# Kernel tuning notes

Hardware: AMD Instinct MI355X
Metric: run time of the kernel (lower is better)

## Reference

```python
import jax, jax.numpy as jnp
from jax import lax
import numpy as np

K = 32          # PyG radius_graph default max_num_neighbors
NEG = -1e9      # mask fill for max-aggregation


def _gather(a, i):  # a [N,C], i [...,] int -> a[i]
    return a[i]


def radius_knn(pos, r):
    # pos [B,N,3] -> (idx [B,N,K], valid [B,N,K]) nearest-K within radius r, self excluded
    sq = jnp.sum(pos * pos, -1)                                   # [B,N]
    d2 = sq[:, :, None] + sq[:, None, :] - 2.0 * jnp.einsum('bnc,bmc->bnm', pos, pos)
    N = pos.shape[1]
    d2 = d2 + jnp.eye(N, dtype=pos.dtype) * 1e9                    # exclude self-loops
    neg, idx = lax.top_k(-d2, K)
    valid = (-neg) <= r * r
    return idx, valid


def fps(pos, n):
    # iterative farthest point sampling, deterministic start at index 0; pos [B,N,3] -> idx [B,n]
    def one(p):
        mind0 = jnp.sum((p - p[0]) ** 2, -1)
        def step(mind, _):
            i = jnp.argmax(mind)
            nd = jnp.sum((p - p[i]) ** 2, -1)
            return jnp.minimum(mind, nd), i
        _, idxs = lax.scan(step, mind0, None, length=n - 1)
        return jnp.concatenate([jnp.zeros((1,), jnp.int32), idxs.astype(jnp.int32)])
    return jax.vmap(one)(pos)


def point_conv(x, pos, idx, valid, W1, b1, W2, b2):
    # PyG PointNetConv: msg = local_nn(concat(x_j, pos_j - pos_i)), max-aggregate
    g = jax.vmap(_gather)
    rel = g(pos, idx) - pos[:, :, None, :]                         # [B,N,K,3]
    feat = rel if x is None else jnp.concatenate([g(x, idx), rel], -1)
    h = jax.nn.relu(feat @ W1 + b1) @ W2 + b2                      # [B,N,K,C]
    h = jnp.where(valid[..., None], h, NEG)
    return jnp.max(h, axis=2)                                      # [B,N,C]


def _forward(pos, W1a, b1a, W1b, b1b, W2a, b2a, W2b, b2b, W3a, b3a, W3b, b3b,
             Wc1, bc1, Wc2, bc2, Wc3, bc3, Wd1, bd1, Wd2, bd2):
    take = jax.vmap(_gather)
    B, N, _ = pos.shape
    idx, v = radius_knn(pos, 0.2)
    x = jax.nn.relu(point_conv(None, pos, idx, v, W1a, b1a, W1b, b1b))
    fi = fps(pos, N // 2)
    x, pos = take(x, fi), take(pos, fi)
    idx, v = radius_knn(pos, 0.4)
    x = jax.nn.relu(point_conv(x, pos, idx, v, W2a, b2a, W2b, b2b))
    fi = fps(pos, N // 8)
    x, pos = take(x, fi), take(pos, fi)
    idx, v = radius_knn(pos, 1.0)
    x = jax.nn.relu(point_conv(x, pos, idx, v, W3a, b3a, W3b, b3b))
    feat = jnp.max(x, axis=1)                                      # global max pool [B,256]
    h = jax.nn.relu(feat @ Wc1 + bc1)
    h = jax.nn.relu(h @ Wc2 + bc2)                                 # dropout is identity in eval
    logits = h @ Wc3 + bc3
    h2 = jax.nn.relu(feat @ Wd1 + bd1)
    d = h2 @ Wd2 + bd2
    return jax.nn.log_softmax(logits, axis=-1), jax.nn.log_softmax(d, axis=-1)


def setup_inputs() -> dict:
    key = jax.random.key(0)
    ks = jax.random.split(key, 32)
    def lin(k, fin, fout):
        kw, kb = jax.random.split(k)
        s = 1.0 / np.sqrt(fin)
        return (jax.random.uniform(kw, (fin, fout), jnp.float32, -s, s),
                jax.random.uniform(kb, (fout,), jnp.float32, -s, s))
    inp = {'pos': jax.random.uniform(ks[0], (8, 4096, 3), jnp.float32)}
    names = [('W1a','b1a',3,64),('W1b','b1b',64,64),('W2a','b2a',67,128),('W2b','b2b',128,128),
             ('W3a','b3a',131,256),('W3b','b3b',256,256),('Wc1','bc1',256,256),('Wc2','bc2',256,256),
             ('Wc3','bc3',256,40),('Wd1','bd1',256,256),('Wd2','bd2',256,2)]
    for i, (wn, bn, fin, fout) in enumerate(names):
        W, b = lin(ks[i + 1], fin, fout)
        inp[wn], inp[bn] = W, b
    return inp


def reference(pos, W1a, b1a, W1b, b1b, W2a, b2a, W2b, b2b, W3a, b3a, W3b, b3b,
              Wc1, bc1, Wc2, bc2, Wc3, bc3, Wd1, bd1, Wd2, bd2):
    return _forward(pos, W1a, b1a, W1b, b1b, W2a, b2a, W2b, b2b, W3a, b3a, W3b, b3b,
                    Wc1, bc1, Wc2, bc2, Wc3, bc3, Wd1, bd1, Wd2, bd2)
```

## Files before the change

### kernel.cpp

```cpp
#include <hip/hip_runtime.h>


#define NB 8

__device__ __forceinline__ unsigned obits(float f) {
  unsigned u = __float_as_uint(f);
  return (u & 0x80000000u) ? ~u : (u | 0x80000000u);
}

static constexpr int CAND = 1024;

template<int CTRL>
__device__ __forceinline__ unsigned long long dpp_max_step(unsigned long long v) {
  const int lo = (int)(unsigned)(v & 0xffffffffull);
  const int hi = (int)(unsigned)(v >> 32);
  const unsigned nlo = (unsigned)__builtin_amdgcn_update_dpp(lo, lo, CTRL, 0xf, 0xf, false);
  const unsigned nhi = (unsigned)__builtin_amdgcn_update_dpp(hi, hi, CTRL, 0xf, 0xf, false);
  const unsigned long long nv = ((unsigned long long)nhi << 32) | nlo;
  return (nv > v) ? nv : v;
}

__device__ __forceinline__ unsigned wave_iscan_add(unsigned x) {
  x += (unsigned)__builtin_amdgcn_update_dpp(0, (int)x, 0x111, 0xf, 0xf, true);
  x += (unsigned)__builtin_amdgcn_update_dpp(0, (int)x, 0x112, 0xf, 0xf, true);
  x += (unsigned)__builtin_amdgcn_update_dpp(0, (int)x, 0x114, 0xf, 0xf, true);
  x += (unsigned)__builtin_amdgcn_update_dpp(0, (int)x, 0x118, 0xf, 0xf, true);
  x += (unsigned)__builtin_amdgcn_update_dpp(0, (int)x, 0x142, 0xa, 0xf, true);
  x += (unsigned)__builtin_amdgcn_update_dpp(0, (int)x, 0x143, 0xc, 0xf, true);
  return x;
}

__device__ __forceinline__ unsigned long long u64max(unsigned long long a,
                                                    unsigned long long b) {
  return (b > a) ? b : a;
}

__device__ __forceinline__ void set_wave_prio_hi() {
#if __has_builtin(__builtin_amdgcn_s_setprio)
  __builtin_amdgcn_s_setprio(3);
#endif
}

template<int N, int NOUT, int T>
__device__ __forceinline__ void fps_body(char* sm, const float* __restrict__ pb,
                                         int* __restrict__ fi, int b) {
  constexpr int P = N / T;
  constexpr int NW = T / 64;
  int4* sPosI = (int4*)sm;
  int*  sfi   = (int*)(sm + (size_t)N * 16);
  unsigned long long* sKey =
      (unsigned long long*)(sm + (size_t)N * 16 + NOUT * 4);
  const int tid = threadIdx.x, wid = tid >> 6, lane = tid & 63;
  set_wave_prio_hi();
  int ix[P], iy[P], iz[P];
  unsigned long long mind[P];
  for (int t = tid; t < N; t += T) {
    sPosI[t] = make_int4((int)(pb[3*t]   * 8388608.f),
                         (int)(pb[3*t+1] * 8388608.f),
                         (int)(pb[3*t+2] * 8388608.f), 0);
  }
  __syncthreads();
  const int x0 = sPosI[0].x, y0 = sPosI[0].y, z0 = sPosI[0].z;
  const int invBase = 4095 - tid * P;
  unsigned long long bv;
  {
    unsigned long long tv[P];
#pragma unroll
    for (int e = 0; e < P; e++) {
      const int j = tid * P + e;
      const int4 p4 = sPosI[j];
      ix[e] = p4.x; iy[e] = p4.y; iz[e] = p4.z;
      const long long dx = p4.x - x0, dy = p4.y - y0, dz = p4.z - z0;
      const unsigned long long d2 =
          (unsigned long long)(dx * dx + dy * dy + dz * dz);
      const unsigned long long k = (d2 << 12) | (unsigned)(invBase - e);
      mind[e] = k; tv[e] = k;
    }
#pragma unroll
    for (int s = 1; s < P; s <<= 1)
#pragma unroll
      for (int e = 0; e + s < P; e += 2 * s)
        if (tv[e + s] > tv[e]) tv[e] = tv[e + s];
    bv = tv[0];
  }
  if (tid == 0) sfi[0] = 0;
  for (int t = 1; t < NOUT; t++) {
    unsigned long long v = bv;
    v = dpp_max_step<0x111>(v);
    v = dpp_max_step<0x112>(v);
    v = dpp_max_step<0x114>(v);
    v = dpp_max_step<0x118>(v);
    v = dpp_max_step<0x142>(v);
    v = dpp_max_step<0x143>(v);
    const int pp = t & 1;
    if (lane == 63) sKey[pp * NW + wid] = v;
    __syncthreads();
    unsigned long long best;
    if (NW == 8) {
      unsigned long long k0 = sKey[pp*8+0], k1 = sKey[pp*8+1],
                         k2 = sKey[pp*8+2], k3 = sKey[pp*8+3],
                         k4 = sKey[pp*8+4], k5 = sKey[pp*8+5],
                         k6 = sKey[pp*8+6], k7 = sKey[pp*8+7];
      k0 = u64max(k0, k1); k2 = u64max(k2, k3);
      k4 = u64max(k4, k5); k6 = u64max(k6, k7);
      k0 = u64max(k0, k2); k4 = u64max(k4, k6);
      best = u64max(k0, k4);
    } else {
      unsigned long long k0 = sKey[pp*NW+0];
#pragma unroll
      for (int w2 = 1; w2 < NW; w2++) k0 = u64max(k0, sKey[pp*NW+w2]);
      best = k0;
    }
    const int ii = 4095 - (int)(best & 0xFFFull);
    if (tid == 0) sfi[t] = ii;
    const int4 wc = sPosI[ii];
    unsigned long long tv[P];
#pragma unroll
    for (int e = 0; e < P; e++) {
      const long long dx = ix[e] - wc.x, dy = iy[e] - wc.y, dz = iz[e] - wc.z;
      const unsigned long long nd =
          (unsigned long long)(dx * dx + dy * dy + dz * dz);
      const unsigned long long nk = (nd << 12) | (unsigned)(invBase - e);
      unsigned long long mk = mind[e];
      mk = (nk < mk) ? nk : mk;
      mind[e] = mk;
      tv[e] = mk;
    }
#pragma unroll
    for (int s = 1; s < P; s <<= 1)
#pragma unroll
      for (int e = 0; e + s < P; e += 2 * s)
        if (tv[e + s] > tv[e]) tv[e] = tv[e + s];
    bv = tv[0];
  }
  __syncthreads();
  for (int t = tid; t < NOUT; t += T) fi[(size_t)b * NOUT + t] = sfi[t];
}

template<int N, int H, int C, bool HASX, bool FOLDMAX, int T>
__device__ __forceinline__ void knnconv_body(
    char* sm, const float* __restrict__ pb, int b, int i,
    const float* __restrict__ U, const float* __restrict__ Wrel,
    const float* __restrict__ b1, const float* __restrict__ W2,
    const float* __restrict__ b2, float* __restrict__ out, double rr) {
  constexpr int HCHUNK = (C == 64) ? 64 : (C == 128 ? 32 : 16);
  constexpr int STR = HCHUNK + 4;
  constexpr int NW = T / 64;
  constexpr int EPK = 32 / NW;
  constexpr int BPT = 2048 / T;
  constexpr int KNNFRONT = N * 8 + 13312;
  constexpr int CONVFRONT = 32 * H * 4 + C * STR * 4 + NW * C * 4;
  constexpr int FRONT = (KNNFRONT > CONVFRONT) ? KNNFRONT : CONVFRONT;
  double*   d2s     = (double*)sm;
  unsigned* hist    = (unsigned*)(sm + N * 8);
  int*      candIdx = (int*)(sm + N * 8 + 8192);
  unsigned* sWT     = (unsigned*)(sm + N * 8 + 12288);
  float* h1s  = (float*)sm;
  float* sW2T = (float*)(sm + 32 * H * 4);
  float* sRed = (float*)(sm + 32 * H * 4 + C * STR * 4);
  int*   snbr = (int*)(sm + FRONT);
  float* rel  = (float*)(sm + FRONT + 128);
  int*   pcnt = (int*)(sm + FRONT + 128 + 384);
  int*   pbin = pcnt + 1;
  const int tid = threadIdx.x;

  const double xi = pb[3*i], yi = pb[3*i+1], zi = pb[3*i+2];
  const double si = (xi*xi + yi*yi) + zi*zi;
  for (int t = tid; t < 2048; t += T) hist[t] = 0u;
  if (tid == 0) *pcnt = 0;
  __syncthreads();
  for (int j = tid; j < N; j += T) {
    double xj = pb[3*j], yj = pb[3*j+1], zj = pb[3*j+2];
    double sj = (xj*xj + yj*yj) + zj*zj;
    double dt = (xi*xj + yi*yj) + zi*zj;
    double d2 = (si + sj) - 2.0*dt;
    if (j == i) d2 += 1e9;
    d2s[j] = d2;
    atomicAdd(&hist[obits((float)d2) >> 21], 1u);
  }
  __syncthreads();
  unsigned lsum = 0;
  const int base = tid * BPT;
#pragma unroll
  for (int q = 0; q < BPT; q++) lsum += hist[base + q];
  const unsigned isc = wave_iscan_add(lsum);
  if ((tid & 63) == 63) sWT[tid >> 6] = isc;
  __syncthreads();
  {
    const int wid = tid >> 6;
    unsigned offs = 0;
#pragma unroll
    for (int w2 = 0; w2 < NW; w2++) offs += (w2 < wid) ? sWT[w2] : 0u;
    const unsigned incl = isc + offs, excl = incl - lsum;
    if (excl < 32u && incl >= 32u) {
      unsigned c = excl;
      for (int q = 0; q < BPT; q++) {
        c += hist[base + q];
        if (c >= 32u) { *pbin = base + q; break; }
      }
    }
  }
  __syncthreads();
  const int binT = *pbin;
  for (int j = tid; j < N; j += T) {
    if ((int)(obits((float)d2s[j]) >> 21) <= binT) {
      int p = atomicAdd(pcnt, 1);
      if (p < CAND) candIdx[p] = j;
    }
  }
  __syncthreads();
  const int M = min(*pcnt, CAND);
  for (int c = tid; c < M; c += T) {
    const int j = candIdx[c];
    const double d = d2s[j];
    int rank = 0;
    for (int e = 0; e < M; e++) {
      const int j2 = candIdx[e];
      const double de = d2s[j2];
      rank += (de < d || (de == d && j2 < j)) ? 1 : 0;
    }
    if (rank < 32) snbr[rank] = (d <= rr) ? j : -1;
  }
  __syncthreads();

  if (tid < 32) {
    const int j = snbr[tid];
    float rx = 0.f, ry = 0.f, rz = 0.f;
    if (j >= 0) {
      rx = pb[3*j]   - pb[3*i];
      ry = pb[3*j+1] - pb[3*i+1];
      rz = pb[3*j+2] - pb[3*i+2];
    }
    rel[tid*3+0] = rx; rel[tid*3+1] = ry; rel[tid*3+2] = rz;
  }
  __syncthreads();

  constexpr int QPK = H / 4;
  for (int qi = tid; qi < 32 * QPK; qi += T) {
    const int k = qi / QPK, h0 = (qi - k * QPK) * 4;
    const int j = snbr[k];
    float4 v = make_float4(0.f, 0.f, 0.f, 0.f);
    if (j >= 0) {
      float4 a = HASX ? *(const float4*)&U[((size_t)b * N + j) * H + h0]
                      : *(const float4*)&b1[h0];
      const float rx = rel[k*3], ry = rel[k*3+1], rz = rel[k*3+2];
      const float4 w0 = *(const float4*)&Wrel[h0];
      const float4 w1 = *(const float4*)&Wrel[H + h0];
      const float4 w2 = *(const float4*)&Wrel[2 * H + h0];
      a.x += rx * w0.x + ry * w1.x + rz * w2.x;
      a.y += rx * w0.y + ry * w1.y + rz * w2.y;
      a.z += rx * w0.z + ry * w1.z + rz * w2.z;
      a.w += rx * w0.w + ry * w1.w + rz * w2.w;
      v = make_float4(fmaxf(a.x, 0.f), fmaxf(a.y, 0.f),
                      fmaxf(a.z, 0.f), fmaxf(a.w, 0.f));
    }
    *(float4*)&h1s[k * H + h0] = v;
  }
  const int cc = tid & 63;
  const int kk = tid >> 6;
  constexpr int CC = C / 64;
  float acc[EPK][CC];
#pragma unroll
  for (int e = 0; e < EPK; e++)
#pragma unroll
    for (int q = 0; q < CC; q++) acc[e][q] = 0.f;
  for (int hc = 0; hc < H; hc += HCHUNK) {
    __syncthreads();
    for (int idx = tid; idx < HCHUNK * C; idx += T) {
      const int hh = idx / C, c = idx - hh * C;
      sW2T[c * STR + hh] = W2[(size_t)(hc + hh) * C + c];
    }
    __syncthreads();
    for (int hh0 = 0; hh0 < HCHUNK; hh0 += 4) {
      float4 wv[CC];
#pragma unroll
      for (int q = 0; q < CC; q++)
        wv[q] = *(const float4*)&sW2T[(cc + q * 64) * STR + hh0];
#pragma unroll
      for (int e = 0; e < EPK; e++) {
        const float4 hv = *(const float4*)&h1s[(kk + e * NW) * H + hc + hh0];
#pragma unroll
        for (int q = 0; q < CC; q++) {
          acc[e][q] += hv.x * wv[q].x;
          acc[e][q] += hv.y * wv[q].y;
          acc[e][q] += hv.z * wv[q].z;
          acc[e][q] += hv.w * wv[q].w;
        }
      }
    }
  }
  float m[CC];
#pragma unroll
  for (int q = 0; q < CC; q++) m[q] = -1e9f;
#pragma unroll
  for (int e = 0; e < EPK; e++) {
    if (snbr[kk + e * NW] >= 0) {
#pragma unroll
      for (int q = 0; q < CC; q++) m[q] = fmaxf(m[q], acc[e][q]);
    }
  }
#pragma unroll
  for (int q = 0; q < CC; q++) sRed[kk * C + cc + q * 64] = m[q];
  __syncthreads();
  if (kk == 0) {
#pragma unroll
    for (int q = 0; q < CC; q++) {
      const int c = cc + q * 64;
      float mm = sRed[c];
#pragma unroll
      for (int w2 = 1; w2 < NW; w2++) mm = fmaxf(mm, sRed[w2 * C + c]);
      const float o = (mm > -5e8f) ? (mm + b2[c]) : -1e9f;
      const float r = fmaxf(o, 0.f);
      if (FOLDMAX) {
        atomicMax((int*)&out[b * C + c], __float_as_int(r));
      } else {
        out[((size_t)b * N + i) * C + c] = r;
      }
    }
  }
}

template<int N, int NOUT, int H, int C, bool HASX, int SMSIZE>
__device__ __forceinline__ void stage_fused_impl(
    const float* pos, double rr, int* fi, const float* U, const float* Wrel,
    const float* b1, const float* W2, const float* b2, float* out, char* sm) {
  if (blockIdx.x < NB) {
    fps_body<N, NOUT, 512>(sm, pos + (size_t)blockIdx.x * N * 3, fi, blockIdx.x);
  } else {
    const int row = blockIdx.x - NB;
    const int b = row / N;
    const int i = row - b * N;
    knnconv_body<N, H, C, HASX, false, 512>(sm, pos + (size_t)b * N * 3, b, i,
                                            U, Wrel, b1, W2, b2, out, rr);
  }
}

__global__ __launch_bounds__(512, 2)
void stage1_kernel(const float* __restrict__ pos, double rr, int* __restrict__ fi,
                   const float* __restrict__ Wrel, const float* __restrict__ b1,
                   const float* __restrict__ W2, const float* __restrict__ b2,
                   float* __restrict__ out) {
  __shared__ __align__(16) char sm[73856];
  stage_fused_impl<4096, 2048, 64, 64, false, 73856>(
      pos, rr, fi, nullptr, Wrel, b1, W2, b2, out, sm);
}

__global__ __launch_bounds__(512, 2)
void stage2_kernel(const float* __restrict__ pos, double rr, int* __restrict__ fi,
                   const float* __restrict__ U, const float* __restrict__ Wrel,
                   const float* __restrict__ b1, const float* __restrict__ W2,
                   const float* __restrict__ b2, float* __restrict__ out) {
  __shared__ __align__(16) char sm[39440];
  stage_fused_impl<2048, 512, 128, 128, true, 39440>(
      pos, rr, fi, U, Wrel, b1, W2, b2, out, sm);
}

__global__ __launch_bounds__(512)
void stage3_kernel(const float* __restrict__ pos, double rr,
                   const float* __restrict__ U, const float* __restrict__ Wrel,
                   const float* __restrict__ b1, const float* __restrict__ W2,
                   const float* __restrict__ b2, float* __restrict__ feat) {
  __shared__ __align__(16) char sm[61968];
  const int b = blockIdx.x / 512;
  const int i = blockIdx.x - b * 512;
  knnconv_body<512, 256, 256, true, true, 512>(sm, pos + (size_t)b * 512 * 3,
                                               b, i, U, Wrel, b1, W2, b2,
                                               feat, rr);
}

template<int CIN, int HH>
__global__ __launch_bounds__(HH)
void gp_kernel(const float* __restrict__ X, const float* __restrict__ posPrev,
               const int* __restrict__ fi, int Nprev, int M,
               const float* __restrict__ W, const float* __restrict__ bias,
               float* __restrict__ U, float* __restrict__ posDst) {
  const int row = blockIdx.x;
  const int b = row / M;
  const int tid = threadIdx.x;
  const int j = fi[row];
  __shared__ float sx[CIN];
  if (tid < CIN) sx[tid] = X[((size_t)b * Nprev + j) * CIN + tid];
  if (tid < 3) posDst[(size_t)row * 3 + tid] = posPrev[((size_t)b * Nprev + j) * 3 + tid];
  __syncthreads();
  float a = bias[tid];
  for (int f = 0; f < CIN; f++) a = fmaf(sx[f], W[f * HH + tid], a);
  U[(size_t)row * HH + tid] = a;
}

__global__ __launch_bounds__(256) void head_kernel(
    const float* __restrict__ feat,
    const float* __restrict__ Wc1, const float* __restrict__ bc1,
    const float* __restrict__ Wc2, const float* __restrict__ bc2,
    const float* __restrict__ Wc3, const float* __restrict__ bc3,
    const float* __restrict__ Wd1, const float* __restrict__ bd1,
    const float* __restrict__ Wd2, const float* __restrict__ bd2,
    float* __restrict__ out) {
  const int b = blockIdx.x, tid = threadIdx.x;
  __shared__ float sf[256], sh[256], sh2[256], shd[256], sl[48];
  sf[tid] = feat[b * 256 + tid];
  __syncthreads();
  float a = bc1[tid], ad = bd1[tid];
  for (int f = 0; f < 256; f++) {
    const float fv = sf[f];
    a  = fmaf(fv, Wc1[f * 256 + tid], a);
    ad = fmaf(fv, Wd1[f * 256 + tid], ad);
  }
  sh[tid] = fmaxf(a, 0.f);
  shd[tid] = fmaxf(ad, 0.f);
  __syncthreads();
  float a2 = bc2[tid];
  for (int f = 0; f < 256; f++) a2 = fmaf(sh[f], Wc2[f * 256 + tid], a2);
  sh2[tid] = fmaxf(a2, 0.f);
  __syncthreads();
  if (tid < 40) {
    float l = bc3[tid];
    for (int f = 0; f < 256; f++) l = fmaf(sh2[f], Wc3[f * 40 + tid], l);
    sl[tid] = l;
  }
  if (tid >= 64 && tid < 66) {
    const int q = tid - 64;
    float l = bd2[q];
    for (int f = 0; f < 256; f++) l = fmaf(shd[f], Wd2[f * 2 + q], l);
    sl[40 + q] = l;
  }
  __syncthreads();
  if (tid == 0) {
    float m0 = sl[0];
    for (int q = 1; q < 40; q++) m0 = fmaxf(m0, sl[q]);
    float s = 0.f;
    for (int q = 0; q < 40; q++) s += expf(sl[q] - m0);
    const float ls = logf(s);
    for (int q = 0; q < 40; q++) out[b * 40 + q] = sl[q] - m0 - ls;
    const float m1 = fmaxf(sl[40], sl[41]);
    const float s1 = expf(sl[40] - m1) + expf(sl[41] - m1);
    const float ls1 = logf(s1);
    out[320 + b * 2 + 0] = sl[40] - m1 - ls1;
    out[320 + b * 2 + 1] = sl[41] - m1 - ls1;
  }
}

extern "C" void kernel_launch(void* const* d_in, const int* in_sizes, int n_in,
                              void* d_out, int out_size, void* d_ws, size_t ws_size,
                              hipStream_t stream) {
  (void)in_sizes; (void)n_in; (void)out_size; (void)ws_size;
  const float* pos = (const float*)d_in[0];
  const float* W1a = (const float*)d_in[1];  const float* b1a = (const float*)d_in[2];
  const float* W1b = (const float*)d_in[3];  const float* b1b = (const float*)d_in[4];
  const float* W2a = (const float*)d_in[5];  const float* b2a = (const float*)d_in[6];
  const float* W2b = (const float*)d_in[7];  const float* b2b = (const float*)d_in[8];
  const float* W3a = (const float*)d_in[9];  const float* b3a = (const float*)d_in[10];
  const float* W3b = (const float*)d_in[11]; const float* b3b = (const float*)d_in[12];
  const float* Wc1 = (const float*)d_in[13]; const float* bc1 = (const float*)d_in[14];
  const float* Wc2 = (const float*)d_in[15]; const float* bc2 = (const float*)d_in[16];
  const float* Wc3 = (const float*)d_in[17]; const float* bc3 = (const float*)d_in[18];
  const float* Wd1 = (const float*)d_in[19]; const float* bd1 = (const float*)d_in[20];
  const float* Wd2 = (const float*)d_in[21]; const float* bd2 = (const float*)d_in[22];
  float* out = (float*)d_out;

  char* w = (char*)d_ws;
  auto alloc = [&](size_t bytes) -> void* {
    void* p = (void*)w;
    w += (bytes + 255) & ~(size_t)255;
    return p;
  };
  int*   fi1  = (int*)  alloc((size_t)NB*2048*4);
  float* x1   = (float*)alloc((size_t)NB*4096*64*4);
  float* pos2 = (float*)alloc((size_t)NB*2048*3*4);
  float* U2   = (float*)alloc((size_t)NB*2048*128*4);
  float* x2   = (float*)alloc((size_t)NB*2048*128*4);
  int*   fi2  = (int*)  alloc((size_t)NB*512*4);
  float* pos3 = (float*)alloc((size_t)NB*512*3*4);
  float* U3   = (float*)alloc((size_t)NB*512*256*4);
  float* feat = (float*)alloc((size_t)NB*256*4);

  hipMemsetAsync(feat, 0, (size_t)NB * 256 * 4, stream);

  stage1_kernel<<<NB + NB * 4096, 512, 0, stream>>>(
      pos, 0.2 * 0.2, fi1, W1a, b1a, W1b, b1b, x1);

  gp_kernel<64, 128><<<NB * 2048, 128, 0, stream>>>(
      x1, pos, fi1, 4096, 2048, W2a, b2a, U2, pos2);

  stage2_kernel<<<NB + NB * 2048, 512, 0, stream>>>(
      pos2, 0.4 * 0.4, fi2, U2, W2a + (size_t)64 * 128, b2a, W2b, b2b, x2);

  gp_kernel<128, 256><<<NB * 512, 256, 0, stream>>>(
      x2, pos2, fi2, 2048, 512, W3a, b3a, U3, pos3);

  stage3_kernel<<<NB * 512, 512, 0, stream>>>(
      pos3, 1.0, U3, W3a + (size_t)128 * 256, b3a, W3b, b3b, feat);

  head_kernel<<<NB, 256, 0, stream>>>(feat, Wc1, bc1, Wc2, bc2, Wc3, bc3,
                                      Wd1, bd1, Wd2, bd2, out);
}
```

Baseline: 2.585 ms.

## Spatially bin FPS points per thread and skip distance updates via bounding-box bound

Before iterating, farthest point sampling now sorts points into a coarse spatial grid with a histogram, prefix scan and scatter, so each thread owns a spatially compact set of points. Each thread keeps the bounding box of its points. On each iteration it skips the distance-update loop when the box's lower-bound distance to the new centroid cannot beat its current maximum min-distance. This cuts per-iteration ALU work on the serial FPS critical path, at the cost of a sorting preamble, extra shared memory, and divergent skipping within waves.

```diff
diff --git a/kernel.cpp b/kernel.cpp
--- a/kernel.cpp
+++ b/kernel.cpp
@@ -46,34 +46,98 @@
                                          int* __restrict__ fi, int b) {
   constexpr int P = N / T;
   constexpr int NW = T / 64;
+  constexpr int CELLS = (N >= 4096) ? 512 : 256;
+  constexpr int CZB = (CELLS == 512) ? 3 : 2;
+  constexpr int CH = NOUT;
+  constexpr int NCHUNK = N / CH;
+  static_assert(CH % P == 0 && N % CH == 0, "chunking");
   int4* sPosI = (int4*)sm;
   int*  sfi   = (int*)(sm + (size_t)N * 16);
   unsigned long long* sKey =
       (unsigned long long*)(sm + (size_t)N * 16 + NOUT * 4);
+  unsigned* hist = (unsigned*)(sm + (size_t)N * 16 + NOUT * 4 + 128);
+  int* sOrd = sfi;
   const int tid = threadIdx.x, wid = tid >> 6, lane = tid & 63;
   set_wave_prio_hi();
-  int ix[P], iy[P], iz[P];
-  unsigned long long mind[P];
+
   for (int t = tid; t < N; t += T) {
     sPosI[t] = make_int4((int)(pb[3*t]   * 8388608.f),
                          (int)(pb[3*t+1] * 8388608.f),
                          (int)(pb[3*t+2] * 8388608.f), 0);
   }
-  __syncthreads();
-  const int x0 = sPosI[0].x, y0 = sPosI[0].y, z0 = sPosI[0].z;
-  const int invBase = 4095 - tid * P;
+  for (int c = tid; c < CELLS; c += T) hist[c] = 0u;
+  __syncthreads();
+
+  unsigned myc[P];
+#pragma unroll
+  for (int r = 0; r < P; r++) {
+    const int t = tid + r * T;
+    const int4 p4 = sPosI[t];
+    const unsigned cell = (((unsigned)p4.x >> 20) << (3 + CZB)) |
+                          (((unsigned)p4.y >> 20) << CZB) |
+                          ((unsigned)p4.z >> (23 - CZB));
+    myc[r] = cell;
+    atomicAdd(&hist[cell], 1u);
+  }
+  __syncthreads();
+
+  {
+    unsigned* sPart = (unsigned*)sKey;
+    unsigned v = (tid < CELLS) ? hist[tid] : 0u;
+    const unsigned isc = wave_iscan_add(v);
+    if (lane == 63) sPart[wid] = isc;
+    __syncthreads();
+    unsigned offs = 0;
+#pragma unroll
+    for (int w2 = 0; w2 < NW; w2++) offs += (w2 < wid) ? sPart[w2] : 0u;
+    if (tid < CELLS) hist[tid] = offs + isc - v;
+    __syncthreads();
+  }
+
+  int myslot[P];
+#pragma unroll
+  for (int r = 0; r < P; r++) myslot[r] = (int)atomicAdd(&hist[myc[r]], 1u);
+
+  int ex[P], ey[P], ez[P]; unsigned einv[P];
+  for (int pc = 0; pc < NCHUNK; pc++) {
+    __syncthreads();
+#pragma unroll
+    for (int r = 0; r < P; r++) {
+      const int s = myslot[r];
+      if (s >= pc * CH && s < (pc + 1) * CH) sOrd[s - pc * CH] = tid + r * T;
+    }
+    __syncthreads();
+    if ((tid * P) / CH == pc) {
+#pragma unroll
+      for (int e = 0; e < P; e++) {
+        const int o = sOrd[tid * P + e - pc * CH];
+        const int4 p4 = sPosI[o];
+        ex[e] = p4.x; ey[e] = p4.y; ez[e] = p4.z;
+        einv[e] = (unsigned)(4095 - o);
+      }
+    }
+  }
+  __syncthreads();
+
+  int lox = ex[0], hix = ex[0], loy = ey[0], hiy = ey[0], loz = ez[0], hiz = ez[0];
+#pragma unroll
+  for (int e = 1; e < P; e++) {
+    lox = min(lox, ex[e]); hix = max(hix, ex[e]);
+    loy = min(loy, ey[e]); hiy = max(hiy, ey[e]);
+    loz = min(loz, ez[e]); hiz = max(hiz, ez[e]);
+  }
+
+  const int4 p0 = sPosI[0];
+  unsigned long long mind[P];
   unsigned long long bv;
   {
     unsigned long long tv[P];
 #pragma unroll
     for (int e = 0; e < P; e++) {
-      const int j = tid * P + e;
-      const int4 p4 = sPosI[j];
-      ix[e] = p4.x; iy[e] = p4.y; iz[e] = p4.z;
-      const long long dx = p4.x - x0, dy = p4.y - y0, dz = p4.z - z0;
+      const long long dx = ex[e] - p0.x, dy = ey[e] - p0.y, dz = ez[e] - p0.z;
       const unsigned long long d2 =
           (unsigned long long)(dx * dx + dy * dy + dz * dz);
-      const unsigned long long k = (d2 << 12) | (unsigned)(invBase - e);
+      const unsigned long long k = (d2 << 12) | einv[e];
       mind[e] = k; tv[e] = k;
     }
 #pragma unroll
@@ -84,6 +148,7 @@
     bv = tv[0];
   }
   if (tid == 0) sfi[0] = 0;
+
   for (int t = 1; t < NOUT; t++) {
     unsigned long long v = bv;
     v = dpp_max_step<0x111>(v);
@@ -114,24 +179,34 @@
     const int ii = 4095 - (int)(best & 0xFFFull);
     if (tid == 0) sfi[t] = ii;
     const int4 wc = sPosI[ii];
-    unsigned long long tv[P];
-#pragma unroll
-    for (int e = 0; e < P; e++) {
-      const long long dx = ix[e] - wc.x, dy = iy[e] - wc.y, dz = iz[e] - wc.z;
-      const unsigned long long nd =
-          (unsigned long long)(dx * dx + dy * dy + dz * dz);
-      const unsigned long long nk = (nd << 12) | (unsigned)(invBase - e);
-      unsigned long long mk = mind[e];
-      mk = (nk < mk) ? nk : mk;
-      mind[e] = mk;
-      tv[e] = mk;
-    }
-#pragma unroll
-    for (int s = 1; s < P; s <<= 1)
-#pragma unroll
-      for (int e = 0; e + s < P; e += 2 * s)
-        if (tv[e + s] > tv[e]) tv[e] = tv[e + s];
-    bv = tv[0];
+
+    const int ax = max(max(lox - wc.x, wc.x - hix), 0);
+    const int ay = max(max(loy - wc.y, wc.y - hiy), 0);
+    const int az = max(max(loz - wc.z, wc.z - hiz), 0);
+    const unsigned long long lb =
+        (unsigned long long)ax * (unsigned long long)ax +
+        (unsigned long long)ay * (unsigned long long)ay +
+        (unsigned long long)az * (unsigned long long)az;
+    if (lb < (bv >> 12)) {
+      unsigned long long tv[P];
+#pragma unroll
+      for (int e = 0; e < P; e++) {
+        const long long dx = ex[e] - wc.x, dy = ey[e] - wc.y, dz = ez[e] - wc.z;
+        const unsigned long long nd =
+            (unsigned long long)(dx * dx + dy * dy + dz * dz);
+        const unsigned long long nk = (nd << 12) | einv[e];
+        unsigned long long mk = mind[e];
+        mk = (nk < mk) ? nk : mk;
+        mind[e] = mk;
+        tv[e] = mk;
+      }
+#pragma unroll
+      for (int s = 1; s < P; s <<= 1)
+#pragma unroll
+        for (int e = 0; e + s < P; e += 2 * s)
+          if (tv[e + s] > tv[e]) tv[e] = tv[e + s];
+      bv = tv[0];
+    }
   }
   __syncthreads();
   for (int t = tid; t < NOUT; t += T) fi[(size_t)b * NOUT + t] = sfi[t];
@@ -340,8 +415,8 @@
                    const float* __restrict__ Wrel, const float* __restrict__ b1,
                    const float* __restrict__ W2, const float* __restrict__ b2,
                    float* __restrict__ out) {
-  __shared__ __align__(16) char sm[73856];
-  stage_fused_impl<4096, 2048, 64, 64, false, 73856>(
+  __shared__ __align__(16) char sm[75904];
+  stage_fused_impl<4096, 2048, 64, 64, false, 75904>(
       pos, rr, fi, nullptr, Wrel, b1, W2, b2, out, sm);
 }
 
```

Measured after the change: 2.358 ms. 8.8% less time.
